# Optimization experiments

Hardware: AMD Instinct MI355X
Metric: run time of the kernel (lower is better)

## Reference

```python
import jax, jax.numpy as jnp
import numpy as np

N_NODES = 50000
N_EDGES = 800000
IN_DIM = 256
HID = 32
HEADS = 8
N_CLASSES = 40
NEG_SLOPE = 0.2  # DGL GATConv default


def setup_inputs() -> dict:
    key = jax.random.key(0)
    ks = jax.random.split(key, 9)
    x = jax.random.normal(ks[0], (N_NODES, IN_DIM), dtype=jnp.float32)
    src = jax.random.randint(ks[1], (N_EDGES,), 0, N_NODES)
    dst = jax.random.randint(ks[2], (N_EDGES,), 0, N_NODES)
    s = 0.05
    W1 = jax.random.normal(ks[3], (IN_DIM, HEADS * HID), dtype=jnp.float32) * s
    al1 = jax.random.normal(ks[4], (HEADS, HID), dtype=jnp.float32) * s
    ar1 = jax.random.normal(ks[5], (HEADS, HID), dtype=jnp.float32) * s
    W2 = jax.random.normal(ks[6], (HEADS * HID, N_CLASSES), dtype=jnp.float32) * s
    al2 = jax.random.normal(ks[7], (1, N_CLASSES), dtype=jnp.float32) * s
    ar2 = jax.random.normal(ks[8], (1, N_CLASSES), dtype=jnp.float32) * s
    return {"x": x, "src": src, "dst": dst, "W1": W1, "al1": al1, "ar1": ar1,
            "W2": W2, "al2": al2, "ar2": ar2}


def gat_conv(h, src, dst, W, al, ar, heads, dout):
    # h: [N, F_in]; W: [F_in, heads*dout]; al/ar: [heads, dout]
    feat = (h @ W).reshape(-1, heads, dout)               # [N, H, D]
    el = (feat * al).sum(-1)                               # [N, H]
    er = (feat * ar).sum(-1)                               # [N, H]
    e = jax.nn.leaky_relu(el[src] + er[dst], NEG_SLOPE)    # [E, H]
    # segment softmax over incoming edges of each dst node
    emax = jax.ops.segment_max(e, dst, num_segments=N_NODES)
    emax = lax_stop(jnp.where(jnp.isfinite(emax), emax, 0.0))
    ee = jnp.exp(e - emax[dst])                            # [E, H]
    denom = jax.ops.segment_sum(ee, dst, num_segments=N_NODES)
    alpha = ee / denom[dst]                                # [E, H]
    msg = feat[src] * alpha[:, :, None]                    # [E, H, D]
    return jax.ops.segment_sum(msg, dst, num_segments=N_NODES)  # [N, H, D]


def lax_stop(v):
    return jax.lax.stop_gradient(v)


def reference(x, src, dst, W1, al1, ar1, W2, al2, ar2):
    # eval mode: feat dropout is identity
    h = gat_conv(x, src, dst, W1, al1, ar1, HEADS, HID)    # [N, 8, 32]
    h = jax.nn.relu(h.reshape(N_NODES, HEADS * HID))       # flatten(1) + relu
    h = gat_conv(h, src, dst, W2, al2, ar2, 1, N_CLASSES)  # [N, 1, C]
    h = h.mean(axis=1)                                     # [N, C]
    return jax.nn.log_softmax(h, axis=1)
```

## Files before the change

kernel.cpp:

```cpp
#include <hip/hip_runtime.h>
#include <hip/hip_bf16.h>
#include <math.h>

#define N_NODES 50000
#define N_EDGES 800000
#define IN_DIM  256
#define HID     32
#define HEADS   8
#define NCLS    40
#define NEG     0.2f
#define CAP1    128
#define CAP2    128

using short8  = __attribute__((ext_vector_type(8))) short;
using f32x4   = __attribute__((ext_vector_type(4))) float;
using floatx2 = __attribute__((ext_vector_type(2))) float;

__device__ __forceinline__ float leaky(float x) { return x >= 0.f ? x : NEG * x; }
__device__ __forceinline__ unsigned short f2b(float f) {
    unsigned int u = __float_as_uint(f);
    unsigned int r = (u + 0x7fffu + ((u >> 16) & 1u)) >> 16;
    return (unsigned short)r;
}
__device__ __forceinline__ float b2f(unsigned short h) {
    return __uint_as_float((unsigned int)h << 16);
}


__global__ void cvt_hist_k(const float* __restrict__ W1, const float* __restrict__ W2,
                           unsigned short* __restrict__ BTile, unsigned short* __restrict__ W2T,
                           const int* __restrict__ dst, int* __restrict__ deg) {
    if (blockIdx.x < 256) {
        int n = blockIdx.x, k = threadIdx.x;
        BTile[(size_t)(k >> 5) * 8192 + n * 32 + (k & 31)] = f2b(W1[k * 256 + n]);
        if (n < 48) {
            int half = k >> 7, cs = (k & 127) >> 3, ni = k & 7;
            int ck = half * 128 + ni * 16 + cs;
            W2T[n * 256 + k] = (n < 40) ? f2b(W2[ck * 40 + n]) : (unsigned short)0;
        }
    } else {
        int e4 = (blockIdx.x - 256) * 256 + threadIdx.x;
        if (e4 * 4 >= N_EDGES) return;
        int4 d = *reinterpret_cast<const int4*>(dst + e4 * 4);
        atomicAdd(&deg[d.x], 1);
        atomicAdd(&deg[d.y], 1);
        atomicAdd(&deg[d.z], 1);
        atomicAdd(&deg[d.w], 1);
    }
}

__global__ __launch_bounds__(256) void gemm1_mfma(const float* __restrict__ A,
                                                  const unsigned short* __restrict__ BTile,
                                                  unsigned char* __restrict__ F8, int M) {
    __shared__ unsigned short Asm[2][64][40];
    __shared__ unsigned short Bsm[2][256][40];
    int t = threadIdx.x;
    int lane = t & 63, w = t >> 6;
    int wr = w >> 1, wc = w & 1;
    int m0 = blockIdx.x * 64;
    int rsub = lane & 15, koff = (lane >> 4) * 8;
    f32x4 acc[2][8] = {};

    int ar = t >> 2, ac = (t & 3) * 8;
    const float* ap = A + (size_t)(m0 + ar) * 256 + ac;
    bool aok = (m0 + ar) < M;
    const unsigned short* bp = BTile + (size_t)t * 32;

    float4 a0 = make_float4(0.f, 0.f, 0.f, 0.f), a1 = a0;
    if (aok) { a0 = *reinterpret_cast<const float4*>(ap); a1 = *reinterpret_cast<const float4*>(ap + 4); }
    uint4 b0 = *reinterpret_cast<const uint4*>(bp);
    uint4 b1 = *reinterpret_cast<const uint4*>(bp + 8);
    uint4 b2 = *reinterpret_cast<const uint4*>(bp + 16);
    uint4 b3 = *reinterpret_cast<const uint4*>(bp + 24);
    {
        short8 bb;
        bb[0] = (short)f2b(a0.x); bb[1] = (short)f2b(a0.y); bb[2] = (short)f2b(a0.z); bb[3] = (short)f2b(a0.w);
        bb[4] = (short)f2b(a1.x); bb[5] = (short)f2b(a1.y); bb[6] = (short)f2b(a1.z); bb[7] = (short)f2b(a1.w);
        *reinterpret_cast<short8*>(&Asm[0][ar][ac]) = bb;
        *reinterpret_cast<uint4*>(&Bsm[0][t][0])  = b0;
        *reinterpret_cast<uint4*>(&Bsm[0][t][8])  = b1;
        *reinterpret_cast<uint4*>(&Bsm[0][t][16]) = b2;
        *reinterpret_cast<uint4*>(&Bsm[0][t][24]) = b3;
    }
    __syncthreads();

    for (int kt = 0; kt < 8; ++kt) {
        if (kt < 7) {
            a0 = make_float4(0.f, 0.f, 0.f, 0.f); a1 = a0;
            if (aok) {
                const float* p = ap + (kt + 1) * 32;
                a0 = *reinterpret_cast<const float4*>(p);
                a1 = *reinterpret_cast<const float4*>(p + 4);
            }
            const unsigned short* nb = bp + (size_t)(kt + 1) * 8192;
            b0 = *reinterpret_cast<const uint4*>(nb);
            b1 = *reinterpret_cast<const uint4*>(nb + 8);
            b2 = *reinterpret_cast<const uint4*>(nb + 16);
            b3 = *reinterpret_cast<const uint4*>(nb + 24);
        }
        short8 a[2], b[8];
#pragma unroll
        for (int mi = 0; mi < 2; mi++)
            a[mi] = *reinterpret_cast<const short8*>(&Asm[kt & 1][wr * 32 + mi * 16 + rsub][koff]);
#pragma unroll
        for (int ni = 0; ni < 8; ni++)
            b[ni] = *reinterpret_cast<const short8*>(&Bsm[kt & 1][wc * 128 + ni * 16 + rsub][koff]);
#pragma unroll
        for (int mi = 0; mi < 2; mi++)
#pragma unroll
            for (int ni = 0; ni < 8; ni++)
                acc[mi][ni] = __builtin_amdgcn_mfma_f32_16x16x32_bf16(a[mi], b[ni], acc[mi][ni], 0, 0, 0);
        if (kt < 7) {
            int nb2 = (kt + 1) & 1;
            short8 bb;
            bb[0] = (short)f2b(a0.x); bb[1] = (short)f2b(a0.y); bb[2] = (short)f2b(a0.z); bb[3] = (short)f2b(a0.w);
            bb[4] = (short)f2b(a1.x); bb[5] = (short)f2b(a1.y); bb[6] = (short)f2b(a1.z); bb[7] = (short)f2b(a1.w);
            *reinterpret_cast<short8*>(&Asm[nb2][ar][ac]) = bb;
            *reinterpret_cast<uint4*>(&Bsm[nb2][t][0])  = b0;
            *reinterpret_cast<uint4*>(&Bsm[nb2][t][8])  = b1;
            *reinterpret_cast<uint4*>(&Bsm[nb2][t][16]) = b2;
            *reinterpret_cast<uint4*>(&Bsm[nb2][t][24]) = b3;
            __syncthreads();
        }
    }

    int rgrp = (lane >> 4) * 4, csub = lane & 15;
#pragma unroll
    for (int mi = 0; mi < 2; mi++) {
#pragma unroll
        for (int i = 0; i < 4; i++) {
            int r = m0 + wr * 32 + mi * 16 + rgrp + i;
            if (r < M) {
                int d0 = __builtin_amdgcn_cvt_pk_fp8_f32(acc[mi][0][i], acc[mi][1][i], 0, false);
                d0 = __builtin_amdgcn_cvt_pk_fp8_f32(acc[mi][2][i], acc[mi][3][i], d0, true);
                int d1 = __builtin_amdgcn_cvt_pk_fp8_f32(acc[mi][4][i], acc[mi][5][i], 0, false);
                d1 = __builtin_amdgcn_cvt_pk_fp8_f32(acc[mi][6][i], acc[mi][7][i], d1, true);
                uint2 st; st.x = (unsigned)d0; st.y = (unsigned)d1;
                *reinterpret_cast<uint2*>(F8 + (size_t)r * 256 + wc * 128 + csub * 8) = st;
            }
        }
    }
}

__global__ __launch_bounds__(256) void elr1_k(const unsigned char* __restrict__ feat8,
                                              const float* __restrict__ al,
                                              const float* __restrict__ ar,
                                              float* __restrict__ el, float* __restrict__ er) {
    int wid = (blockIdx.x * blockDim.x + threadIdx.x) >> 6;
    int lane = threadIdx.x & 63;
    if (wid >= N_NODES) return;
    unsigned u = *reinterpret_cast<const unsigned*>(feat8 + (size_t)wid * 256 + 4 * lane);
    floatx2 lo = __builtin_amdgcn_cvt_pk_f32_fp8((int)u, false);
    floatx2 hi = __builtin_amdgcn_cvt_pk_f32_fp8((int)u, true);
    int csub = (lane & 31) >> 1;
    int h0 = (lane >> 5) * 4 + 2 * (lane & 1);
    float pl0 = lo.x * al[h0 * 32 + csub] + lo.y * al[h0 * 32 + 16 + csub];
    float pr0 = lo.x * ar[h0 * 32 + csub] + lo.y * ar[h0 * 32 + 16 + csub];
    float pl1 = hi.x * al[(h0 + 1) * 32 + csub] + hi.y * al[(h0 + 1) * 32 + 16 + csub];
    float pr1 = hi.x * ar[(h0 + 1) * 32 + csub] + hi.y * ar[(h0 + 1) * 32 + 16 + csub];
#pragma unroll
    for (int d = 2; d <= 16; d <<= 1) {
        pl0 += __shfl_xor(pl0, d); pr0 += __shfl_xor(pr0, d);
        pl1 += __shfl_xor(pl1, d); pr1 += __shfl_xor(pr1, d);
    }
    if (csub == 0) {
        el[wid * 8 + h0] = pl0; el[wid * 8 + h0 + 1] = pl1;
        er[wid * 8 + h0] = pr0; er[wid * 8 + h0 + 1] = pr1;
    }
}

__global__ __launch_bounds__(256) void gemm2_mfma(const unsigned short* __restrict__ A,
                                                  const unsigned short* __restrict__ BT,
                                                  const float* __restrict__ al2,
                                                  const float* __restrict__ ar2,
                                                  unsigned short* __restrict__ C,
                                                  float* __restrict__ el2,
                                                  float* __restrict__ er2, int M) {
    __shared__ unsigned short Asm[2][64][40];
    int t = threadIdx.x;
    int lane = t & 63, w = t >> 6;
    int m0 = blockIdx.x * 64;
    int rsub = lane & 15, koff = (lane >> 4) * 8;
    f32x4 acc[3] = {};

    int r_t = t >> 2, c8 = (t & 3) * 8;
    const unsigned short* ap = A + (size_t)(m0 + r_t) * 256 + c8;
    bool arow_ok = (m0 + r_t) < M;

    uint4 s0 = make_uint4(0, 0, 0, 0);
    if (arow_ok) s0 = *reinterpret_cast<const uint4*>(ap);
    *reinterpret_cast<uint4*>(&Asm[0][r_t][c8]) = s0;
    __syncthreads();

    for (int kt = 0; kt < 8; ++kt) {
        if (kt < 7) {
            s0 = make_uint4(0, 0, 0, 0);
            if (arow_ok) s0 = *reinterpret_cast<const uint4*>(ap + (kt + 1) * 32);
        }
        short8 b[3], a;
#pragma unroll
        for (int ni = 0; ni < 3; ni++)
            b[ni] = *reinterpret_cast<const short8*>(BT + (size_t)(ni * 16 + rsub) * 256 + kt * 32 + koff);
        a = *reinterpret_cast<const short8*>(&Asm[kt & 1][w * 16 + rsub][koff]);
#pragma unroll
        for (int ni = 0; ni < 3; ni++)
            acc[ni] = __builtin_amdgcn_mfma_f32_16x16x32_bf16(a, b[ni], acc[ni], 0, 0, 0);
        if (kt < 7) {
            *reinterpret_cast<uint4*>(&Asm[(kt + 1) & 1][r_t][c8]) = s0;
            __syncthreads();
        }
    }

    int rgrp = (lane >> 4) * 4, csub = lane & 15;
    float alc[3], arc[3];
#pragma unroll
    for (int ni = 0; ni < 3; ni++) {
        int col = ni * 16 + csub;
        alc[ni] = (col < 40) ? al2[col] : 0.f;
        arc[ni] = (col < 40) ? ar2[col] : 0.f;
    }
#pragma unroll
    for (int i = 0; i < 4; i++) {
        int r = m0 + w * 16 + rgrp + i;
        float pl = acc[0][i] * alc[0] + acc[1][i] * alc[1] + acc[2][i] * alc[2];
        float pr = acc[0][i] * arc[0] + acc[1][i] * arc[1] + acc[2][i] * arc[2];
        pl += __shfl_xor(pl, 1); pl += __shfl_xor(pl, 2);
        pl += __shfl_xor(pl, 4); pl += __shfl_xor(pl, 8);
        pr += __shfl_xor(pr, 1); pr += __shfl_xor(pr, 2);
        pr += __shfl_xor(pr, 4); pr += __shfl_xor(pr, 8);
        if (r < M) {
#pragma unroll
            for (int ni = 0; ni < 3; ni++) {
                int col = ni * 16 + csub;
                if (col < 40) C[(size_t)r * 40 + col] = f2b(acc[ni][i]);
            }
            if (csub == 0) { el2[r] = pl; er2[r] = pr; }
        }
    }
}

__global__ void scan1_k(const int* __restrict__ deg, int* __restrict__ offs,
                        int* __restrict__ bsum, int n) {
    __shared__ int s[256];
    int tid = threadIdx.x;
    int i = blockIdx.x * 256 + tid;
    int v = (i < n) ? deg[i] : 0;
    s[tid] = v;
    __syncthreads();
    for (int d = 1; d < 256; d <<= 1) {
        int t = (tid >= d) ? s[tid - d] : 0;
        __syncthreads();
        s[tid] += t;
        __syncthreads();
    }
    if (i < n) offs[i] = s[tid] - v;
    if (tid == 255) bsum[blockIdx.x] = s[255];
}

__global__ void scan3_k(int* __restrict__ offs, const int* __restrict__ bsum,
                        int* __restrict__ cur, int n, int nb) {
    __shared__ int red[256];
    int tid = threadIdx.x;
    int v = (tid < blockIdx.x && tid < nb) ? bsum[tid] : 0;
    red[tid] = v;
    __syncthreads();
#pragma unroll
    for (int d = 128; d > 0; d >>= 1) {
        if (tid < d) red[tid] += red[tid + d];
        __syncthreads();
    }
    int prefix = red[0];
    int i = blockIdx.x * 256 + tid;
    if (i < n) { offs[i] += prefix; cur[i] = 0; }
    if (i == 0) offs[n] = N_EDGES;
}

__global__ void scatter_k(const int* __restrict__ src, const int* __restrict__ dst,
                          const int* __restrict__ offs, int* __restrict__ cur,
                          int* __restrict__ ssorted) {
    int e4 = blockIdx.x * blockDim.x + threadIdx.x;
    if (e4 * 4 >= N_EDGES) return;
    int4 d = *reinterpret_cast<const int4*>(dst + e4 * 4);
    int4 sv = *reinterpret_cast<const int4*>(src + e4 * 4);
    int p;
    p = atomicAdd(&cur[d.x], 1); ssorted[offs[d.x] + p] = sv.x;
    p = atomicAdd(&cur[d.y], 1); ssorted[offs[d.y] + p] = sv.y;
    p = atomicAdd(&cur[d.z], 1); ssorted[offs[d.z] + p] = sv.z;
    p = atomicAdd(&cur[d.w], 1); ssorted[offs[d.w] + p] = sv.w;
}

__global__ __launch_bounds__(256) void agg1_k(const unsigned char* __restrict__ feat8,
                                              const float* __restrict__ el,
                                              const float* __restrict__ er,
                                              const int* __restrict__ offs,
                                              const int* __restrict__ ssorted,
                                              unsigned short* __restrict__ h1) {
    __shared__ float sa[4][CAP1 * 8];
    __shared__ int   ss[4][CAP1];
    int t = threadIdx.x;
    int wv = t >> 6, lane = t & 63;
    int n = blockIdx.x * 4 + wv;
    if (n >= N_NODES) return;
    int beg = offs[n];
    int deg = offs[n + 1] - beg;
    int eloc = lane >> 3, h = lane & 7;
    int h0 = (lane >> 5) * 4 + 2 * (lane & 1);
    float er_h = er[n * 8 + h];

    float acc0 = 0.f, acc1 = 0.f, acc2 = 0.f, acc3 = 0.f;

    if (deg <= CAP1) {
        float ssum = 0.f;
        int c0 = 0;
        for (; c0 + 32 <= deg; c0 += 32) {
#pragma unroll
            for (int q = 0; q < 4; q++) {
                int idx = c0 + q * 8 + eloc;
                int s = ssorted[beg + idx];
                if (h == 0) ss[wv][idx] = s;
                float ee = __expf(leaky(el[s * 8 + h] + er_h));
                sa[wv][idx * 8 + h] = ee;
                ssum += ee;
            }
        }
        for (; c0 < deg; c0 += 8) {
            int idx = c0 + eloc;
            if (idx < deg) {
                int s = ssorted[beg + idx];
                if (h == 0) ss[wv][idx] = s;
                float ee = __expf(leaky(el[s * 8 + h] + er_h));
                sa[wv][idx * 8 + h] = ee;
                ssum += ee;
            }
        }
        ssum += __shfl_xor(ssum, 8);
        ssum += __shfl_xor(ssum, 16);
        ssum += __shfl_xor(ssum, 32);
        float inv = 1.f / ssum;
        float iv0 = __shfl(inv, h0), iv1 = __shfl(inv, h0 + 1);
        asm volatile("s_waitcnt lgkmcnt(0)" ::: "memory");
        for (c0 = 0; c0 < deg; c0 += 32) {
            int nr = deg - c0; if (nr > 32) nr = 32;
            unsigned u[32];
#pragma unroll
            for (int j = 0; j < 32; j++) {
                if (j < nr) {
                    int sj = ss[wv][c0 + j];
                    u[j] = *reinterpret_cast<const unsigned*>(feat8 + (size_t)sj * 256 + 4 * lane);
                }
            }
#pragma unroll
            for (int j = 0; j < 32; j++) {
                if (j < nr) {
                    float2 av = *reinterpret_cast<const float2*>(&sa[wv][(c0 + j) * 8 + h0]);
                    floatx2 lo = __builtin_amdgcn_cvt_pk_f32_fp8((int)u[j], false);
                    floatx2 hi = __builtin_amdgcn_cvt_pk_f32_fp8((int)u[j], true);
                    acc0 += av.x * lo.x;
                    acc1 += av.x * lo.y;
                    acc2 += av.y * hi.x;
                    acc3 += av.y * hi.y;
                }
            }
        }
        acc0 *= iv0; acc1 *= iv0; acc2 *= iv1; acc3 *= iv1;
    } else {
        float ssum = 0.f;
        for (int c0 = 0; c0 < deg; c0 += 8) {
            bool act = (c0 + eloc) < deg;
            float ee = 0.f;
            if (act) {
                int s = ssorted[beg + c0 + eloc];
                ee = __expf(leaky(el[s * 8 + h] + er_h));
            }
            ssum += ee;
        }
        ssum += __shfl_xor(ssum, 8);
        ssum += __shfl_xor(ssum, 16);
        ssum += __shfl_xor(ssum, 32);
        float inv = 1.f / ssum;
        float iv0 = __shfl(inv, h0), iv1 = __shfl(inv, h0 + 1);
        for (int c0 = 0; c0 < deg; c0 += 8) {
            int nr = deg - c0; if (nr > 8) nr = 8;
            int s = 0; float a = 0.f;
            if (eloc < nr) {
                s = ssorted[beg + c0 + eloc];
                a = __expf(leaky(el[s * 8 + h] + er_h));
            }
#pragma unroll
            for (int j = 0; j < 8; j++) {
                if (j < nr) {
                    int   sj = __shfl(s, j * 8);
                    float a0 = __shfl(a, j * 8 + h0) * iv0;
                    float a1 = __shfl(a, j * 8 + h0 + 1) * iv1;
                    unsigned u = *reinterpret_cast<const unsigned*>(feat8 + (size_t)sj * 256 + 4 * lane);
                    floatx2 lo = __builtin_amdgcn_cvt_pk_f32_fp8((int)u, false);
                    floatx2 hi = __builtin_amdgcn_cvt_pk_f32_fp8((int)u, true);
                    acc0 += a0 * lo.x;
                    acc1 += a0 * lo.y;
                    acc2 += a1 * hi.x;
                    acc3 += a1 * hi.y;
                }
            }
        }
    }
    ushort4 o;
    o.x = f2b(fmaxf(acc0, 0.f));
    o.y = f2b(fmaxf(acc1, 0.f));
    o.z = f2b(fmaxf(acc2, 0.f));
    o.w = f2b(fmaxf(acc3, 0.f));
    *reinterpret_cast<ushort4*>(h1 + (size_t)n * 256 + 4 * lane) = o;
}

__global__ __launch_bounds__(256) void agg2_k(const unsigned short* __restrict__ feat2q,
                                              const float* __restrict__ el2,
                                              const float* __restrict__ er2,
                                              const int* __restrict__ offs,
                                              const int* __restrict__ ssorted,
                                              float* __restrict__ out) {
    __shared__ float sa[4][CAP2];
    __shared__ int   ss[4][CAP2];
    int t = threadIdx.x;
    int wv = t >> 6, lane = t & 63;
    int n = blockIdx.x * 4 + wv;
    if (n >= N_NODES) return;
    int beg = offs[n];
    int deg = offs[n + 1] - beg;
    float ern = er2[n];
    int eloc = lane >> 3, c8 = lane & 7;

    float acc[8] = {};
    if (deg <= CAP2) {
        float ssum = 0.f;
        for (int c0 = 0; c0 < deg; c0 += 64) {
            int idx = c0 + lane;
            if (idx < deg) {
                int s = ssorted[beg + idx];
                ss[wv][idx] = s;
                float ee = __expf(leaky(el2[s] + ern));
                sa[wv][idx] = ee;
                ssum += ee;
            }
        }
#pragma unroll
        for (int d = 1; d < 64; d <<= 1) ssum += __shfl_xor(ssum, d);
        float inv = 1.f / ssum;
        asm volatile("s_waitcnt lgkmcnt(0)" ::: "memory");
        for (int c0 = 0; c0 < deg; c0 += 32) {
            uint4 v[4]; float wgt[4];
#pragma unroll
            for (int q = 0; q < 4; q++) {
                int idx = c0 + q * 8 + eloc;
                v[q] = make_uint4(0, 0, 0, 0); wgt[q] = 0.f;
                if (c8 < 5 && idx < deg) {
                    int s = ss[wv][idx]; wgt[q] = sa[wv][idx];
                    v[q] = *reinterpret_cast<const uint4*>(feat2q + (size_t)s * 40 + c8 * 8);
                }
            }
#pragma unroll
            for (int q = 0; q < 4; q++) {
                const unsigned short* pv = reinterpret_cast<const unsigned short*>(&v[q]);
#pragma unroll
                for (int i = 0; i < 8; i++) acc[i] += wgt[q] * b2f(pv[i]);
            }
        }
#pragma unroll
        for (int i = 0; i < 8; i++) acc[i] *= inv;
    } else {
        float ssum = 0.f;
        for (int c0 = 0; c0 < deg; c0 += 64) {
            bool act = (c0 + lane) < deg;
            if (act) ssum += __expf(leaky(el2[ssorted[beg + c0 + lane]] + ern));
        }
#pragma unroll
        for (int d = 1; d < 64; d <<= 1) ssum += __shfl_xor(ssum, d);
        float inv = 1.f / ssum;
        for (int c0 = 0; c0 < deg; c0 += 8) {
            int nr = deg - c0; if (nr > 8) nr = 8;
            if (eloc < nr && c8 < 5) {
                int s = ssorted[beg + c0 + eloc];
                float a = __expf(leaky(el2[s] + ern)) * inv;
                uint4 v = *reinterpret_cast<const uint4*>(feat2q + (size_t)s * 40 + c8 * 8);
                const unsigned short* pv = reinterpret_cast<const unsigned short*>(&v);
#pragma unroll
                for (int i = 0; i < 8; i++) acc[i] += a * b2f(pv[i]);
            }
        }
    }
#pragma unroll
    for (int i = 0; i < 8; i++) {
        acc[i] += __shfl_xor(acc[i], 8);
        acc[i] += __shfl_xor(acc[i], 16);
        acc[i] += __shfl_xor(acc[i], 32);
    }
    float lmax = -INFINITY;
    if (c8 < 5) {
#pragma unroll
        for (int i = 0; i < 8; i++) lmax = fmaxf(lmax, acc[i]);
    }
    lmax = fmaxf(lmax, __shfl_xor(lmax, 1));
    lmax = fmaxf(lmax, __shfl_xor(lmax, 2));
    lmax = fmaxf(lmax, __shfl_xor(lmax, 4));
    float lsum = 0.f;
    if (c8 < 5) {
#pragma unroll
        for (int i = 0; i < 8; i++) lsum += __expf(acc[i] - lmax);
    }
    lsum += __shfl_xor(lsum, 1);
    lsum += __shfl_xor(lsum, 2);
    lsum += __shfl_xor(lsum, 4);
    if (eloc == 0 && c8 < 5) {
        float lg = __logf(lsum);
        float* o = out + (size_t)n * 40 + c8 * 8;
#pragma unroll
        for (int i = 0; i < 8; i++) o[i] = acc[i] - lmax - lg;
    }
}

extern "C" void kernel_launch(void* const* d_in, const int* in_sizes, int n_in,
                              void* d_out, int out_size, void* d_ws, size_t ws_size,
                              hipStream_t stream) {
    (void)in_sizes; (void)n_in; (void)out_size; (void)ws_size;
    const float* x   = (const float*)d_in[0];
    const int*   src = (const int*)d_in[1];
    const int*   dst = (const int*)d_in[2];
    const float* W1  = (const float*)d_in[3];
    const float* al1 = (const float*)d_in[4];
    const float* ar1 = (const float*)d_in[5];
    const float* W2  = (const float*)d_in[6];
    const float* al2 = (const float*)d_in[7];
    const float* ar2 = (const float*)d_in[8];
    float* out = (float*)d_out;

    char* ws = (char*)d_ws;
    size_t off = 0;
    auto alloc = [&](size_t bytes) {
        void* p = ws + off;
        off += (bytes + 255) & ~(size_t)255;
        return p;
    };
    unsigned short* w1tile = (unsigned short*)alloc((size_t)8 * 256 * 32 * 2);
    unsigned short* w2t    = (unsigned short*)alloc((size_t)48 * 256 * 2);
    unsigned char*  feat8  = (unsigned char*)alloc((size_t)N_NODES * 256);
    unsigned short* h1p    = (unsigned short*)alloc((size_t)N_NODES * 256 * 2);
    unsigned short* feat2q = (unsigned short*)alloc((size_t)N_NODES * 40 * 2);
    float* el1   = (float*)alloc((size_t)N_NODES * 8 * 4);
    float* er1   = (float*)alloc((size_t)N_NODES * 8 * 4);
    float* el2   = (float*)alloc((size_t)N_NODES * 4);
    float* er2   = (float*)alloc((size_t)N_NODES * 4);
    int* deg     = (int*)alloc((size_t)N_NODES * 4);
    int* offs    = (int*)alloc((size_t)(N_NODES + 1) * 4);
    int* cur     = (int*)alloc((size_t)N_NODES * 4);
    int* bsum    = (int*)alloc(1024 * 4);
    int* ssorted = (int*)alloc((size_t)N_EDGES * 4);

    hipMemsetAsync(deg, 0, (size_t)N_NODES * 4, stream);

    cvt_hist_k<<<256 + (N_EDGES / 4 + 255) / 256, 256, 0, stream>>>(W1, W2, w1tile, w2t, dst, deg);
    int nb = (N_NODES + 255) / 256;
    scan1_k<<<nb, 256, 0, stream>>>(deg, offs, bsum, N_NODES);
    scan3_k<<<nb, 256, 0, stream>>>(offs, bsum, cur, N_NODES, nb);
    scatter_k<<<(N_EDGES / 4 + 255) / 256, 256, 0, stream>>>(src, dst, offs, cur, ssorted);

    gemm1_mfma<<<(N_NODES + 63) / 64, 256, 0, stream>>>(x, w1tile, feat8, N_NODES);
    elr1_k<<<(N_NODES * 64 + 255) / 256, 256, 0, stream>>>(feat8, al1, ar1, el1, er1);
    agg1_k<<<(N_NODES + 3) / 4, 256, 0, stream>>>(feat8, el1, er1, offs, ssorted, h1p);

    gemm2_mfma<<<(N_NODES + 63) / 64, 256, 0, stream>>>(h1p, w2t, al2, ar2, feat2q, el2, er2, N_NODES);
    agg2_k<<<(N_NODES + 3) / 4, 256, 0, stream>>>(feat2q, el2, er2, offs, ssorted, out);
}
```

Measured before the change: 216.3 us.

## Record edge ranks during histogram and fuse atomic-free scatter into GEMM1 launch

The histogram kernel now keeps the return value of each degree atomic as a per-edge rank and stores it to a new array. The scatter then needs no second atomic pass and no cursor reset. The scatter work runs as extra blocks inside the GEMM1 launch, which removes one kernel launch and lets the scatter overlap the GEMM. In exchange the rank array adds an 800K-int write and a later read, and the edge order within each node's list now follows the histogram atomics.

```diff
diff --git a/kernel.cpp b/kernel.cpp
--- a/kernel.cpp
+++ b/kernel.cpp
@@ -29,7 +29,8 @@
 
 __global__ void cvt_hist_k(const float* __restrict__ W1, const float* __restrict__ W2,
                            unsigned short* __restrict__ BTile, unsigned short* __restrict__ W2T,
-                           const int* __restrict__ dst, int* __restrict__ deg) {
+                           const int* __restrict__ dst, int* __restrict__ deg,
+                           int* __restrict__ rank) {
     if (blockIdx.x < 256) {
         int n = blockIdx.x, k = threadIdx.x;
         BTile[(size_t)(k >> 5) * 8192 + n * 32 + (k & 31)] = f2b(W1[k * 256 + n]);
@@ -42,18 +43,38 @@
         int e4 = (blockIdx.x - 256) * 256 + threadIdx.x;
         if (e4 * 4 >= N_EDGES) return;
         int4 d = *reinterpret_cast<const int4*>(dst + e4 * 4);
-        atomicAdd(&deg[d.x], 1);
-        atomicAdd(&deg[d.y], 1);
-        atomicAdd(&deg[d.z], 1);
-        atomicAdd(&deg[d.w], 1);
-    }
-}
-
-__global__ __launch_bounds__(256) void gemm1_mfma(const float* __restrict__ A,
-                                                  const unsigned short* __restrict__ BTile,
-                                                  unsigned char* __restrict__ F8, int M) {
+        int4 rk;
+        rk.x = atomicAdd(&deg[d.x], 1);
+        rk.y = atomicAdd(&deg[d.y], 1);
+        rk.z = atomicAdd(&deg[d.z], 1);
+        rk.w = atomicAdd(&deg[d.w], 1);
+        *reinterpret_cast<int4*>(rank + e4 * 4) = rk;
+    }
+}
+
+__global__ __launch_bounds__(256) void gemm1_scatter_k(const float* __restrict__ A,
+                                                       const unsigned short* __restrict__ BTile,
+                                                       unsigned char* __restrict__ F8, int M,
+                                                       int gblocks,
+                                                       const int* __restrict__ src,
+                                                       const int* __restrict__ dst,
+                                                       const int* __restrict__ rank,
+                                                       const int* __restrict__ offs,
+                                                       int* __restrict__ ssorted) {
     __shared__ unsigned short Asm[2][64][40];
     __shared__ unsigned short Bsm[2][256][40];
+    if (blockIdx.x >= gblocks) {
+        int e4 = (blockIdx.x - gblocks) * 256 + threadIdx.x;
+        if (e4 * 4 >= N_EDGES) return;
+        int4 d  = *reinterpret_cast<const int4*>(dst + e4 * 4);
+        int4 sv = *reinterpret_cast<const int4*>(src + e4 * 4);
+        int4 rk = *reinterpret_cast<const int4*>(rank + e4 * 4);
+        ssorted[offs[d.x] + rk.x] = sv.x;
+        ssorted[offs[d.y] + rk.y] = sv.y;
+        ssorted[offs[d.z] + rk.z] = sv.z;
+        ssorted[offs[d.w] + rk.w] = sv.w;
+        return;
+    }
     int t = threadIdx.x;
     int lane = t & 63, w = t >> 6;
     int wr = w >> 1, wc = w & 1;
@@ -258,7 +279,7 @@
 }
 
 __global__ void scan3_k(int* __restrict__ offs, const int* __restrict__ bsum,
-                        int* __restrict__ cur, int n, int nb) {
+                        int n, int nb) {
     __shared__ int red[256];
     int tid = threadIdx.x;
     int v = (tid < blockIdx.x && tid < nb) ? bsum[tid] : 0;
@@ -271,22 +292,8 @@
     }
     int prefix = red[0];
     int i = blockIdx.x * 256 + tid;
-    if (i < n) { offs[i] += prefix; cur[i] = 0; }
+    if (i < n) offs[i] += prefix;
     if (i == 0) offs[n] = N_EDGES;
-}
-
-__global__ void scatter_k(const int* __restrict__ src, const int* __restrict__ dst,
-                          const int* __restrict__ offs, int* __restrict__ cur,
-                          int* __restrict__ ssorted) {
-    int e4 = blockIdx.x * blockDim.x + threadIdx.x;
-    if (e4 * 4 >= N_EDGES) return;
-    int4 d = *reinterpret_cast<const int4*>(dst + e4 * 4);
-    int4 sv = *reinterpret_cast<const int4*>(src + e4 * 4);
-    int p;
-    p = atomicAdd(&cur[d.x], 1); ssorted[offs[d.x] + p] = sv.x;
-    p = atomicAdd(&cur[d.y], 1); ssorted[offs[d.y] + p] = sv.y;
-    p = atomicAdd(&cur[d.z], 1); ssorted[offs[d.z] + p] = sv.z;
-    p = atomicAdd(&cur[d.w], 1); ssorted[offs[d.w] + p] = sv.w;
 }
 
 __global__ __launch_bounds__(256) void agg1_k(const unsigned char* __restrict__ feat8,
@@ -549,19 +556,21 @@
     float* er2   = (float*)alloc((size_t)N_NODES * 4);
     int* deg     = (int*)alloc((size_t)N_NODES * 4);
     int* offs    = (int*)alloc((size_t)(N_NODES + 1) * 4);
-    int* cur     = (int*)alloc((size_t)N_NODES * 4);
+    int* rank    = (int*)alloc((size_t)N_EDGES * 4);
     int* bsum    = (int*)alloc(1024 * 4);
     int* ssorted = (int*)alloc((size_t)N_EDGES * 4);
 
     hipMemsetAsync(deg, 0, (size_t)N_NODES * 4, stream);
 
-    cvt_hist_k<<<256 + (N_EDGES / 4 + 255) / 256, 256, 0, stream>>>(W1, W2, w1tile, w2t, dst, deg);
+    cvt_hist_k<<<256 + (N_EDGES / 4 + 255) / 256, 256, 0, stream>>>(W1, W2, w1tile, w2t, dst, deg, rank);
     int nb = (N_NODES + 255) / 256;
     scan1_k<<<nb, 256, 0, stream>>>(deg, offs, bsum, N_NODES);
-    scan3_k<<<nb, 256, 0, stream>>>(offs, bsum, cur, N_NODES, nb);
-    scatter_k<<<(N_EDGES / 4 + 255) / 256, 256, 0, stream>>>(src, dst, offs, cur, ssorted);
-
-    gemm1_mfma<<<(N_NODES + 63) / 64, 256, 0, stream>>>(x, w1tile, feat8, N_NODES);
+    scan3_k<<<nb, 256, 0, stream>>>(offs, bsum, N_NODES, nb);
+
+    int gblocks = (N_NODES + 63) / 64;
+    int sblocks = (N_EDGES / 4 + 255) / 256;
+    gemm1_scatter_k<<<gblocks + sblocks, 256, 0, stream>>>(x, w1tile, feat8, N_NODES, gblocks,
+                                                           src, dst, rank, offs, ssorted);
     elr1_k<<<(N_NODES * 64 + 255) / 256, 256, 0, stream>>>(feat8, al1, ar1, el1, er1);
     agg1_k<<<(N_NODES + 3) / 4, 256, 0, stream>>>(feat8, el1, er1, offs, ssorted, h1p);
 
```

Result: faster. 182.1 us (-15.8%).
